# Kernel tuning notes

Measured on AMD Instinct MI355X. Metric: run time of the kernel, lower is better.

## Reference

```python
import jax, jax.numpy as jnp
import numpy as np

IMG_H = 800
IMG_W = 800
LEVEL_HW = [(200, 200), (100, 100), (50, 50), (25, 25), (13, 13)]
SIZES = [32.0, 64.0, 128.0, 256.0, 512.0]
RATIOS = np.array([0.5, 1.0, 2.0])
PRE_NMS = 1000     # rpn_pre_nms_top_n_test
POST_NMS = 1000    # rpn_post_nms_top_n_test
NMS_THRESH = 0.7
MIN_SIZE = 1e-3
BBOX_CLAMP = float(np.log(1000.0 / 16.0))  # torchvision BoxCoder clamp


def _make_anchors():
    """torchvision AnchorGenerator: 3 anchors/location, (h,w,a)-major order."""
    per_level = []
    for (H, W), size in zip(LEVEL_HW, SIZES):
        h_r = np.sqrt(RATIOS)
        w_r = 1.0 / h_r
        ws = w_r * size
        hs = h_r * size
        base = np.round(np.stack([-ws, -hs, ws, hs], axis=1) / 2.0)  # [3,4]
        stride_y = IMG_H // H
        stride_x = IMG_W // W
        shift_x = np.arange(W) * stride_x
        shift_y = np.arange(H) * stride_y
        yy, xx = np.meshgrid(shift_y, shift_x, indexing='ij')
        shifts = np.stack([xx.ravel(), yy.ravel(), xx.ravel(), yy.ravel()], axis=1)
        a = (shifts[:, None, :] + base[None, :, :]).reshape(-1, 4)  # [H*W*3,4]
        per_level.append(jnp.asarray(a, jnp.float32))
    return per_level


def _conv(x, w, b, pad):
    y = jax.lax.conv_general_dilated(
        x, w, window_strides=(1, 1), padding=[(pad, pad), (pad, pad)],
        dimension_numbers=('NCHW', 'OIHW', 'NCHW'))
    return y + b[None, :, None, None]


def _rpn_forward(feats, conv_w, conv_b, cls_w, cls_b, bbox_w, bbox_b):
    anchors_l = _make_anchors()
    boxes_list, scores_list, lvls_list = [], [], []
    for lvl, f in enumerate(feats):
        t = jax.nn.relu(_conv(f, conv_w, conv_b, 1))
        logits = _conv(t, cls_w, cls_b, 0)     # [1,3,H,W]
        deltas = _conv(t, bbox_w, bbox_b, 0)   # [1,12,H,W]
        H, W = f.shape[2], f.shape[3]
        s = logits[0].transpose(1, 2, 0).reshape(-1)                       # (h,w,a)
        d = deltas[0].reshape(3, 4, H, W).transpose(2, 3, 0, 1).reshape(-1, 4)
        k = min(PRE_NMS, s.shape[0])
        topv, topi = jax.lax.top_k(s, k)
        a = anchors_l[lvl][topi]
        dd = d[topi]
        # BoxCoder.decode, weights=(1,1,1,1)
        w_ = a[:, 2] - a[:, 0]
        h_ = a[:, 3] - a[:, 1]
        cx = a[:, 0] + 0.5 * w_
        cy = a[:, 1] + 0.5 * h_
        dx, dy = dd[:, 0], dd[:, 1]
        dw = jnp.minimum(dd[:, 2], BBOX_CLAMP)
        dh = jnp.minimum(dd[:, 3], BBOX_CLAMP)
        pcx = dx * w_ + cx
        pcy = dy * h_ + cy
        pw = jnp.exp(dw) * w_
        ph = jnp.exp(dh) * h_
        bx = jnp.stack([pcx - 0.5 * pw, pcy - 0.5 * ph,
                        pcx + 0.5 * pw, pcy + 0.5 * ph], axis=1)
        boxes_list.append(bx)
        scores_list.append(topv)
        lvls_list.append(jnp.full((k,), float(lvl), jnp.float32))
    boxes = jnp.concatenate(boxes_list)    # [N,4], N=4507
    scores = jnp.concatenate(scores_list)
    lvls = jnp.concatenate(lvls_list)
    # clip to image
    boxes = jnp.stack([boxes[:, 0].clip(0.0, IMG_W), boxes[:, 1].clip(0.0, IMG_H),
                       boxes[:, 2].clip(0.0, IMG_W), boxes[:, 3].clip(0.0, IMG_H)], axis=1)
    valid = ((boxes[:, 2] - boxes[:, 0]) >= MIN_SIZE) & ((boxes[:, 3] - boxes[:, 1]) >= MIN_SIZE)
    # batched NMS: offset boxes per level so cross-level IoU is zero
    off = lvls * (IMG_W + 1.0)
    ob = boxes + off[:, None]
    N = boxes.shape[0]
    order = jnp.argsort(-scores)
    b = ob[order]
    rb = boxes[order]
    s = scores[order]
    v = valid[order]
    area = (b[:, 2] - b[:, 0]) * (b[:, 3] - b[:, 1])
    lt = jnp.maximum(b[:, None, :2], b[None, :, :2])
    rbr = jnp.minimum(b[:, None, 2:], b[None, :, 2:])
    wh = jnp.clip(rbr - lt, 0.0)
    inter = wh[..., 0] * wh[..., 1]
    iou = inter / (area[:, None] + area[None, :] - inter)  # [N,N]
    idxs = jnp.arange(N)
    def body(i, keep):
        sup = keep[i] & (iou[i] > NMS_THRESH) & (idxs > i)
        return keep & ~sup
    keep = jax.lax.fori_loop(0, N, body, v)
    final_scores = jnp.where(keep, s, -jnp.inf)
    _, ki = jax.lax.top_k(final_scores, POST_NMS)
    return rb[ki]  # [POST_NMS, 4] proposals (padded to fixed size)


def setup_inputs() -> dict:
    key = jax.random.key(0)
    ks = jax.random.split(key, 12)
    inp = {}
    for i, (name, (H, W)) in enumerate(zip(['feat0', 'feat1', 'feat2', 'feat3', 'feat4'], LEVEL_HW)):
        inp[name] = jax.random.normal(ks[i], (1, 256, H, W), jnp.float32)
    inp['conv_w'] = jax.random.normal(ks[5], (256, 256, 3, 3), jnp.float32) * 0.02
    inp['conv_b'] = jnp.zeros((256,), jnp.float32)
    inp['cls_w'] = jax.random.normal(ks[6], (3, 256, 1, 1), jnp.float32) * 0.02
    inp['cls_b'] = jnp.zeros((3,), jnp.float32)
    inp['bbox_w'] = jax.random.normal(ks[7], (12, 256, 1, 1), jnp.float32) * 0.02
    inp['bbox_b'] = jnp.zeros((12,), jnp.float32)
    return inp


def reference(feat0, feat1, feat2, feat3, feat4, conv_w, conv_b, cls_w, cls_b, bbox_w, bbox_b):
    feats = [feat0, feat1, feat2, feat3, feat4]
    return _rpn_forward(feats, conv_w, conv_b, cls_w, cls_b, bbox_w, bbox_b)
```

## Files before the change

kernel.cpp:

```cpp
#include <hip/hip_runtime.h>
#include <cmath>

typedef unsigned int u32;
typedef unsigned long long u64;
typedef _Float16 f16;
typedef _Float16 f16x8 __attribute__((ext_vector_type(8)));
typedef float f32x4 __attribute__((ext_vector_type(4)));

typedef __attribute__((address_space(1))) const unsigned int gu32;
typedef __attribute__((address_space(3))) unsigned int lu32;

#define NCAND 4507
#define WORDS 71
#define ROWS_AL (WORDS * 64)
#define TOTS 159882

__constant__ int c_W[5]      = {200, 100, 50, 25, 13};
__constant__ int c_stride[5] = {4, 8, 16, 32, 61};
__constant__ int c_Nl[5]     = {120000, 30000, 7500, 1875, 507};
__constant__ int c_soff[5]   = {0, 120000, 150000, 157500, 159375};
__constant__ int c_k[5]      = {1000, 1000, 1000, 1000, 507};

__constant__ int cv_boff[6]  = {0, 625, 794, 843, 859, 863};

struct DecParams { float b[5][3][4]; };
struct FeatPtrs { const float* p[5]; };

__device__ __forceinline__ u32 flipf(float f) {
    u32 u = __float_as_uint(f);
    return (u & 0x80000000u) ? ~u : (u | 0x80000000u);
}

constexpr size_t AL(size_t x) { return (x + 255) & ~(size_t)255; }
constexpr size_t OFF_WHI    = 0;
constexpr size_t OFF_WLO    = AL(OFF_WHI + 1179648);
constexpr size_t OFF_HEADW  = AL(OFF_WLO + 1179648);
constexpr size_t OFF_HEADB  = AL(OFF_HEADW + 3840 * 4);
constexpr size_t OFF_SCORES = AL(OFF_HEADB + 64);
constexpr size_t OFF_DELTAS = AL(OFF_SCORES + (size_t)TOTS * 4);
constexpr size_t OFF_SBOX   = AL(OFF_DELTAS + (size_t)TOTS * 16);
constexpr size_t OFF_SOB    = AL(OFF_SBOX + (size_t)NCAND * 16);
constexpr size_t OFF_SVAL   = AL(OFF_SOB + (size_t)NCAND * 16);
constexpr size_t OFF_MASK   = AL(OFF_SVAL + (size_t)NCAND * 4);
constexpr size_t OFF_KEEP   = AL(OFF_MASK + (size_t)ROWS_AL * WORDS * 8);
constexpr size_t OFF_GHIST  = AL(OFF_KEEP + WORDS * 8);
constexpr size_t OFF_CNT    = AL(OFF_GHIST + 1280 * 4);
constexpr size_t OFF_KEY    = AL(OFF_CNT + 64);

__global__ __launch_bounds__(256) void k_prep(
    const float* __restrict__ cw, const float* __restrict__ clsw,
    const float* __restrict__ clsb, const float* __restrict__ bw,
    const float* __restrict__ bb, f16* __restrict__ whi, f16* __restrict__ wlo,
    float* __restrict__ headw, float* __restrict__ headb,
    u32* __restrict__ ghist, u32* __restrict__ cnts) {
    int i = blockIdx.x * 256 + threadIdx.x;
    if (i < 589824) {
        int blk = i >> 13;
        int within = i & 8191;
        int co = within >> 5;
        int rem = within & 31;
        int slot = rem >> 3, j = rem & 7;
        int chunk = blk / 9, kk = blk - chunk * 9;
        int ky = kk / 3, kx = kk - ky * 3;
        int g = slot ^ ((co >> 1) & 3);
        int ci = (chunk << 5) | (g << 3) | j;
        float w = cw[(((co << 8) + ci) * 3 + ky) * 3 + kx];
        f16 hi = (f16)w;
        whi[i] = hi;
        wlo[i] = (f16)((w - (float)hi) * 2048.0f);
    }
    if (i < 3840) {
        int h = i >> 8, ci = i & 255;
        headw[i] = (h < 3) ? clsw[h * 256 + ci] : bw[(h - 3) * 256 + ci];
    }
    if (i < 15) headb[i] = (i < 3) ? clsb[i] : bb[i - 3];
    if (i < 1280) ghist[i] = 0;
    if (i < 16) cnts[i] = 0;
}

__global__ __launch_bounds__(512) void k_conv(
    FeatPtrs fp, const f16* __restrict__ whi, const f16* __restrict__ wlo,
    const float* __restrict__ convb, const float* __restrict__ headw,
    const float* __restrict__ headb, float* __restrict__ scores,
    float* __restrict__ deltas) {
    __shared__ float4 smq[4896];
    char* smb = (char*)smq;
    const int tid = threadIdx.x;
    const int lane = tid & 63, wv = tid >> 6;
    const int l15 = lane & 15, l4 = lane >> 4;

    const int bid = blockIdx.x;
    int l = 0;
#pragma unroll
    for (int q = 1; q < 5; q++) if (bid >= cv_boff[q]) l = q;
    const int H = c_W[l], W = H;
    const int soff = c_soff[l];
    const float* __restrict__ in = fp.p[l];
    const int t = bid - cv_boff[l];
    const int tilesx = (W + 7) >> 3;
    const int tx = t % tilesx, ty = t / tilesx;
    const int x0 = tx * 8, y0 = ty * 8;
    const int HW = H * W;

    int rbase0, rbase1, rbase2, rbase3;
    {
        int rr = l15 >> 3;
        rbase0 = (0 + rr) * 640; rbase1 = (2 + rr) * 640;
        rbase2 = (4 + rr) * 640; rbase3 = (6 + rr) * 640;
    }
    int colx0, colx1, colx2;
    {
        int c = lane & 7;
        int p0 = c, p1 = c + 1, p2 = c + 2;
        colx0 = p0 * 64 + ((l4 ^ ((p0 >> 1) & 3)) << 4);
        colx1 = p1 * 64 + ((l4 ^ ((p1 >> 1) & 3)) << 4);
        colx2 = p2 * 64 + ((l4 ^ ((p2 >> 1) & 3)) << 4);
    }
    int bco0 = wv * 32 + l15, bco1 = wv * 32 + 16 + l15;
    const int boff0 = bco0 * 64 + ((l4 ^ ((bco0 >> 1) & 3)) << 4);
    const int boff1 = bco1 * 64 + ((l4 ^ ((bco1 >> 1) & 3)) << 4);

    f32x4 acc1[4][2], acc2[4][2];
#pragma unroll
    for (int mt = 0; mt < 4; mt++)
#pragma unroll
        for (int nt = 0; nt < 2; nt++) {
            acc1[mt][nt] = (f32x4)0.0f;
            acc2[mt][nt] = (f32x4)0.0f;
        }

    auto stagePatch = [&](int chunk) {
        const int c0 = chunk << 5;
        f16* ph = (f16*)smb;
        f16* pl = (f16*)(smb + 6400);
        for (int e = tid; e < 3200; e += 512) {
            int py = e / 320, rem = e - py * 320;
            int px = rem >> 5, ci = rem & 31;
            int gy = y0 - 1 + py, gx = x0 - 1 + px;
            float v = 0.f;
            if (gy >= 0 && gy < H && gx >= 0 && gx < W)
                v = in[(c0 + ci) * HW + gy * W + gx];
            f16 hi = (f16)v;
            int widx = py * 320 + px * 32 + (((ci >> 3) ^ ((px >> 1) & 3)) << 3) + (ci & 7);
            ph[widx] = hi;
            pl[widx] = (f16)((v - (float)hi) * 2048.0f);
        }
    };
    auto issueB = [&](int sidx, int buf) {
        const char* gh = (const char*)whi + (size_t)sidx * 16384;
        const char* gl = (const char*)wlo + (size_t)sidx * 16384;
        char* dh = smb + 12800 + buf * 32768;
        char* dl = dh + 16384;
#pragma unroll
        for (int q = 0; q < 2; q++) {
            int i1 = (wv * 2 + q) * 1024;
            __builtin_amdgcn_global_load_lds((gu32*)(gh + i1 + lane * 16), (lu32*)(dh + i1), 16, 0, 0);
            __builtin_amdgcn_global_load_lds((gu32*)(gl + i1 + lane * 16), (lu32*)(dl + i1), 16, 0, 0);
        }
    };

    stagePatch(0);
    issueB(0, 0);
    __syncthreads();

    for (int chunk = 0; chunk < 8; ++chunk) {
        if (chunk) { stagePatch(chunk); __syncthreads(); }
#pragma unroll
        for (int kk = 0; kk < 9; ++kk) {
            const int s = chunk * 9 + kk;
            const int buf = s & 1;
            if (s < 71) issueB(s + 1, buf ^ 1);
            {
                const int ky = kk / 3, kx = kk - ky * 3;
                const int kyb = ky * 640;
                const int cx = (kx == 0) ? colx0 : (kx == 1) ? colx1 : colx2;
                const char* bh = smb + 12800 + buf * 32768;
                const char* bl = bh + 16384;
                f16x8 ah0 = *(const f16x8*)(smb + rbase0 + kyb + cx);
                f16x8 ah1 = *(const f16x8*)(smb + rbase1 + kyb + cx);
                f16x8 ah2 = *(const f16x8*)(smb + rbase2 + kyb + cx);
                f16x8 ah3 = *(const f16x8*)(smb + rbase3 + kyb + cx);
                f16x8 al0 = *(const f16x8*)(smb + 6400 + rbase0 + kyb + cx);
                f16x8 al1 = *(const f16x8*)(smb + 6400 + rbase1 + kyb + cx);
                f16x8 al2 = *(const f16x8*)(smb + 6400 + rbase2 + kyb + cx);
                f16x8 al3 = *(const f16x8*)(smb + 6400 + rbase3 + kyb + cx);
#pragma unroll
                for (int nt = 0; nt < 2; nt++) {
                    const int bo = nt ? boff1 : boff0;
                    f16x8 vbh = *(const f16x8*)(bh + bo);
                    f16x8 vbl = *(const f16x8*)(bl + bo);
                    acc1[0][nt] = __builtin_amdgcn_mfma_f32_16x16x32_f16(ah0, vbh, acc1[0][nt], 0, 0, 0);
                    acc2[0][nt] = __builtin_amdgcn_mfma_f32_16x16x32_f16(ah0, vbl, acc2[0][nt], 0, 0, 0);
                    acc2[0][nt] = __builtin_amdgcn_mfma_f32_16x16x32_f16(al0, vbh, acc2[0][nt], 0, 0, 0);
                    acc1[1][nt] = __builtin_amdgcn_mfma_f32_16x16x32_f16(ah1, vbh, acc1[1][nt], 0, 0, 0);
                    acc2[1][nt] = __builtin_amdgcn_mfma_f32_16x16x32_f16(ah1, vbl, acc2[1][nt], 0, 0, 0);
                    acc2[1][nt] = __builtin_amdgcn_mfma_f32_16x16x32_f16(al1, vbh, acc2[1][nt], 0, 0, 0);
                    acc1[2][nt] = __builtin_amdgcn_mfma_f32_16x16x32_f16(ah2, vbh, acc1[2][nt], 0, 0, 0);
                    acc2[2][nt] = __builtin_amdgcn_mfma_f32_16x16x32_f16(ah2, vbl, acc2[2][nt], 0, 0, 0);
                    acc2[2][nt] = __builtin_amdgcn_mfma_f32_16x16x32_f16(al2, vbh, acc2[2][nt], 0, 0, 0);
                    acc1[3][nt] = __builtin_amdgcn_mfma_f32_16x16x32_f16(ah3, vbh, acc1[3][nt], 0, 0, 0);
                    acc2[3][nt] = __builtin_amdgcn_mfma_f32_16x16x32_f16(ah3, vbl, acc2[3][nt], 0, 0, 0);
                    acc2[3][nt] = __builtin_amdgcn_mfma_f32_16x16x32_f16(al3, vbh, acc2[3][nt], 0, 0, 0);
                }
            }
            __syncthreads();
        }
    }

    const float INV2048 = 4.8828125e-4f;
    {
        float cb0 = convb[bco0], cb1 = convb[bco1];
#pragma unroll
        for (int mt = 0; mt < 4; mt++)
#pragma unroll
            for (int nt = 0; nt < 2; nt++) {
                float cb = nt ? cb1 : cb0;
#pragma unroll
                for (int r = 0; r < 4; r++) {
                    float tv = acc1[mt][nt][r] + acc2[mt][nt][r] * INV2048 + cb;
                    acc1[mt][nt][r] = tv > 0.f ? tv : 0.f;
                }
            }
    }

    float* part = (float*)smb;
    for (int hc = 0; hc < 15; hc += 3) {
        float hw3[3][2];
#pragma unroll
        for (int h3 = 0; h3 < 3; h3++) {
            hw3[h3][0] = headw[(hc + h3) * 256 + bco0];
            hw3[h3][1] = headw[(hc + h3) * 256 + bco1];
        }
#pragma unroll
        for (int mt = 0; mt < 4; mt++)
#pragma unroll
            for (int r = 0; r < 4; r++) {
                float p0 = 0.f, p1 = 0.f, p2 = 0.f;
#pragma unroll
                for (int nt = 0; nt < 2; nt++) {
                    float tv = acc1[mt][nt][r];
                    p0 = fmaf(hw3[0][nt], tv, p0);
                    p1 = fmaf(hw3[1][nt], tv, p1);
                    p2 = fmaf(hw3[2][nt], tv, p2);
                }
                p0 += __shfl_xor(p0, 1); p0 += __shfl_xor(p0, 2); p0 += __shfl_xor(p0, 4); p0 += __shfl_xor(p0, 8);
                p1 += __shfl_xor(p1, 1); p1 += __shfl_xor(p1, 2); p1 += __shfl_xor(p1, 4); p1 += __shfl_xor(p1, 8);
                p2 += __shfl_xor(p2, 1); p2 += __shfl_xor(p2, 2); p2 += __shfl_xor(p2, 4); p2 += __shfl_xor(p2, 8);
                if (l15 == 0) {
                    int px = mt * 16 + l4 * 4 + r;
                    part[(wv * 64 + px) * 3 + 0] = p0;
                    part[(wv * 64 + px) * 3 + 1] = p1;
                    part[(wv * 64 + px) * 3 + 2] = p2;
                }
            }
        __syncthreads();
        if (tid < 192) {
            int px = tid / 3, h3 = tid % 3;
            int h = hc + h3;
            float sum = 0.f;
#pragma unroll
            for (int g = 0; g < 8; g++) sum += part[(g * 64 + px) * 3 + h3];
            sum += headb[h];
            int gy = y0 + (px >> 3), gx = x0 + (px & 7);
            if (gy < H && gx < W) {
                int pix = gy * W + gx;
                if (h < 3) {
                    scores[soff + pix * 3 + h] = sum;
                } else {
                    int ch2 = h - 3;
                    deltas[((size_t)(soff + pix * 3 + (ch2 >> 2))) * 4 + (ch2 & 3)] = sum;
                }
            }
        }
        __syncthreads();
    }
}

__global__ __launch_bounds__(256) void k_hist(
    const float* __restrict__ scores, u32* __restrict__ ghist) {
    __shared__ u32 lh[1280];
    for (int i = threadIdx.x; i < 1280; i += 256) lh[i] = 0;
    __syncthreads();
    const int gsz = gridDim.x * 256;
    for (int i = blockIdx.x * 256 + threadIdx.x; i < TOTS; i += gsz) {
        int l = (i >= 120000) + (i >= 150000) + (i >= 157500) + (i >= 159375);
        u32 b = flipf(scores[i]) >> 24;
        atomicAdd(&lh[l * 256 + b], 1u);
    }
    __syncthreads();
    for (int i = threadIdx.x; i < 1280; i += 256) {
        u32 v = lh[i];
        if (v) atomicAdd(&ghist[i], v);
    }
}

__global__ __launch_bounds__(512) void k_classify(
    const float* __restrict__ scores, const u32* __restrict__ ghist,
    u64* __restrict__ key, u64* __restrict__ scr1, u32* __restrict__ cnts) {
    __shared__ u32 lh[1280];
    __shared__ u32 sb0[5];
    for (int i = threadIdx.x; i < 1280; i += 512) lh[i] = ghist[i];
    __syncthreads();
    if (threadIdx.x < 4) {
        int l = threadIdx.x;
        u32 m0 = (u32)c_k[l];
        u32 cum = 0;
        for (int b = 255; b >= 0; --b) {
            u32 c = lh[l * 256 + b];
            if (cum + c >= m0) { sb0[l] = (u32)b; break; }
            cum += c;
        }
    }
    __syncthreads();
    const int lane = threadIdx.x & 63;
    const int gsz = gridDim.x * 512;
    for (int i = blockIdx.x * 512 + threadIdx.x; i < TOTS; i += gsz) {
        int l = (i >= 120000) + (i >= 150000) + (i >= 157500) + (i >= 159375);
        u32 il = (u32)(i - c_soff[l]);
        u32 k32 = flipf(scores[i]);
        u32 b = k32 >> 24;
        bool sel = (l == 4) || (b > sb0[l]);
        bool tie = (l < 4) && (b == sb0[l]);
        u64 m1 = __ballot(sel);
        while (m1) {
            int ldr = __builtin_ctzll(m1);
            int lv = __shfl(l, ldr);
            u64 grp = __ballot(sel && (l == lv));
            u32 bs = 0;
            if (lane == ldr) bs = atomicAdd(&cnts[lv], (u32)__popcll(grp));
            bs = __shfl(bs, ldr);
            if (sel && l == lv) {
                u32 slot = bs + (u32)__popcll(grp & ((1ull << lane) - 1ull));
                key[lv * 1000 + slot] = ((u64)(~k32) << 32) | (u64)(((u32)lv << 24) | il);
            }
            m1 &= ~grp;
        }
        u64 m2 = __ballot(tie);
        while (m2) {
            int ldr = __builtin_ctzll(m2);
            int lv = __shfl(l, ldr);
            u64 grp = __ballot(tie && (l == lv));
            u32 bs = 0;
            if (lane == ldr) bs = atomicAdd(&cnts[8 + lv], (u32)__popcll(grp));
            bs = __shfl(bs, ldr);
            if (tie && l == lv) {
                u32 slot = bs + (u32)__popcll(grp & ((1ull << lane) - 1ull));
                scr1[c_soff[lv] + slot] = ((u64)k32 << 32) | (u64)il;
            }
            m2 &= ~grp;
        }
    }
}

__global__ __launch_bounds__(1024) void k_finish(
    const u32* __restrict__ cnts, const u64* __restrict__ key,
    const float* __restrict__ deltas, DecParams P,
    u64* __restrict__ scr1, u64* __restrict__ scr2,
    float* __restrict__ sboxes, float* __restrict__ sob, u32* __restrict__ svalid) {
    __shared__ u64 sk[8192];
    __shared__ u32 hist[256];
    __shared__ u32 tiebuf[2048];
    __shared__ u32 sh_sel, sh_t1, sh_t2, sh_m;
    const int tid = threadIdx.x;
    const int lane = tid & 63;

    for (int l = 0; l < 5; ++l) {
        u32 n = cnts[l];
        int base = l * 1000;
        for (u32 j = tid; j < n; j += 1024) sk[base + j] = key[base + j];
    }
    __syncthreads();

    for (int l = 0; l < 4; ++l) {
        const int off = c_soff[l], base = l * 1000;
        const u32 lshift = (u32)l << 24;
        u32 nsel = cnts[l];
        u32 m = (u32)c_k[l] - nsel;
        u32 n = cnts[8 + l];
        u64* curb = scr1 + off;
        u64* nxtb = scr2 + off;
        if (tid == 0) sh_sel = nsel;
        __syncthreads();
        for (int p = 1; p <= 3; ++p) {
            if (n == m) break;
            const int shift = 56 - 8 * p;
            for (int b = tid; b < 256; b += 1024) hist[b] = 0;
            if (tid == 0) sh_t1 = 0;
            __syncthreads();
            for (u32 j = tid; j < n; j += 1024)
                atomicAdd(&hist[(u32)(curb[j] >> shift) & 255u], 1u);
            __syncthreads();
            if (tid == 0) {
                u32 cum = 0;
                for (int b = 255; b >= 0; --b) {
                    u32 c = hist[b];
                    if (cum + c >= m) { sh_t2 = (u32)b; sh_m = m - cum; break; }
                    cum += c;
                }
            }
            __syncthreads();
            u32 bp = sh_t2; m = sh_m;
            for (u32 j = tid; j < n; j += 1024) {
                u64 e = curb[j];
                u32 b = (u32)(e >> shift) & 255u;
                bool sel = b > bp, tie = (b == bp);
                u64 msk = __ballot(sel);
                if (msk) {
                    int ldr = __builtin_ctzll(msk);
                    u32 bs = 0;
                    if (lane == ldr) bs = atomicAdd(&sh_sel, (u32)__popcll(msk));
                    bs = __shfl(bs, ldr);
                    if (sel) {
                        u32 slot = bs + (u32)__popcll(msk & ((1ull << lane) - 1ull));
                        u32 k32 = (u32)(e >> 32);
                        sk[base + slot] = ((u64)(~k32) << 32) | (u64)(lshift | (u32)(e & 0xFFFFFFu));
                    }
                }
                msk = __ballot(tie);
                if (msk) {
                    int ldr = __builtin_ctzll(msk);
                    u32 bs = 0;
                    if (lane == ldr) bs = atomicAdd(&sh_t1, (u32)__popcll(msk));
                    bs = __shfl(bs, ldr);
                    if (tie) {
                        u32 slot = bs + (u32)__popcll(msk & ((1ull << lane) - 1ull));
                        nxtb[slot] = e;
                    }
                }
            }
            __syncthreads();
            n = sh_t1;
            __syncthreads();
            u64* tmp = curb; curb = nxtb; nxtb = tmp;
        }
        u32 cs = sh_sel;
        if (n == m) {
            for (u32 j = tid; j < n; j += 1024) {
                u64 e = curb[j];
                u32 k32 = (u32)(e >> 32);
                sk[base + cs + j] = ((u64)(~k32) << 32) | (u64)(lshift | (u32)(e & 0xFFFFFFu));
            }
        } else {
            u32 kt = (u32)(curb[0] >> 32);
            u32 nc = n > 2048u ? 2048u : n;
            u32 S = 64; while (S < nc) S <<= 1;
            for (u32 j = tid; j < S; j += 1024) tiebuf[j] = 0xFFFFFFFFu;
            __syncthreads();
            for (u32 j = tid; j < nc; j += 1024) tiebuf[j] = (u32)(curb[j] & 0xFFFFFFu);
            __syncthreads();
            for (u32 ksz = 2; ksz <= S; ksz <<= 1) {
                for (u32 jj = ksz >> 1; jj > 0; jj >>= 1) {
                    for (u32 i2 = tid; i2 < S; i2 += 1024) {
                        u32 ixj = i2 ^ jj;
                        if (ixj > i2) {
                            u32 a = tiebuf[i2], b2 = tiebuf[ixj];
                            bool up = ((i2 & ksz) == 0);
                            if ((a > b2) == up) { tiebuf[i2] = b2; tiebuf[ixj] = a; }
                        }
                    }
                    __syncthreads();
                }
            }
            for (u32 j = tid; j < m; j += 1024)
                sk[base + cs + j] = ((u64)(~kt) << 32) | (u64)(lshift | tiebuf[j]);
        }
        __syncthreads();
    }
    for (int i = tid; i < 8192; i += 1024) if (i >= NCAND) sk[i] = ~0ull;
    __syncthreads();
    for (u32 ksz = 2; ksz <= 8192; ksz <<= 1) {
        for (u32 j = ksz >> 1; j > 0; j >>= 1) {
            for (u32 i = tid; i < 8192; i += 1024) {
                u32 ixj = i ^ j;
                if (ixj > i) {
                    u64 a = sk[i], b = sk[ixj];
                    bool up = ((i & ksz) == 0);
                    if ((a > b) == up) { sk[i] = b; sk[ixj] = a; }
                }
            }
            __syncthreads();
        }
    }
    const float CLAMP = 4.135166556742356f;
    for (int s = tid; s < NCAND; s += 1024) {
        u32 info = (u32)sk[s];
        int l = info >> 24, idx = info & 0xFFFFFF;
        int W = c_W[l], st = c_stride[l];
        int a = idx % 3, pix = idx / 3;
        int x = pix % W, y = pix / W;
        float ax1 = x * st + P.b[l][a][0];
        float ay1 = y * st + P.b[l][a][1];
        float ax2 = x * st + P.b[l][a][2];
        float ay2 = y * st + P.b[l][a][3];
        float w_ = ax2 - ax1, h_ = ay2 - ay1;
        float cx = ax1 + 0.5f * w_, cy = ay1 + 0.5f * h_;
        const float* d = deltas + ((size_t)(c_soff[l] + idx)) * 4;
        float dx = d[0], dy = d[1];
        float dw = fminf(d[2], CLAMP), dh = fminf(d[3], CLAMP);
        float pcx = dx * w_ + cx, pcy = dy * h_ + cy;
        float pw = expf(dw) * w_, ph = expf(dh) * h_;
        float x1 = pcx - 0.5f * pw, y1 = pcy - 0.5f * ph;
        float x2 = pcx + 0.5f * pw, y2 = pcy + 0.5f * ph;
        x1 = fminf(fmaxf(x1, 0.f), 800.f); y1 = fminf(fmaxf(y1, 0.f), 800.f);
        x2 = fminf(fmaxf(x2, 0.f), 800.f); y2 = fminf(fmaxf(y2, 0.f), 800.f);
        u32 vv = (x2 - x1 >= 0.001f && y2 - y1 >= 0.001f) ? 1u : 0u;
        float offv = (float)l * 801.0f;
        sboxes[s * 4 + 0] = x1; sboxes[s * 4 + 1] = y1;
        sboxes[s * 4 + 2] = x2; sboxes[s * 4 + 3] = y2;
        sob[s * 4 + 0] = x1 + offv; sob[s * 4 + 1] = y1 + offv;
        sob[s * 4 + 2] = x2 + offv; sob[s * 4 + 3] = y2 + offv;
        svalid[s] = vv;
    }
}

__global__ __launch_bounds__(256) void k_mask(
    const float* __restrict__ sob, u64* __restrict__ mask) {
    int gid = blockIdx.x * 256 + threadIdx.x;
    const int total = NCAND * WORDS;
    if (gid >= total) return;
    int i = gid / WORDS, w = gid - i * WORDS;
    float bx1 = sob[i * 4], by1 = sob[i * 4 + 1], bx2 = sob[i * 4 + 2], by2 = sob[i * 4 + 3];
    float ai = (bx2 - bx1) * (by2 - by1);
    u64 bits = 0;
    int j0 = w * 64;
    for (int b = 0; b < 64; b++) {
        int j = j0 + b;
        if (j < NCAND && j > i) {
            float cx1 = sob[j * 4], cy1 = sob[j * 4 + 1], cx2 = sob[j * 4 + 2], cy2 = sob[j * 4 + 3];
            float lt0 = fmaxf(bx1, cx1), lt1 = fmaxf(by1, cy1);
            float rb0 = fminf(bx2, cx2), rb1 = fminf(by2, cy2);
            float ww = fmaxf(rb0 - lt0, 0.f), hh = fmaxf(rb1 - lt1, 0.f);
            float inter = ww * hh;
            float aj = (cx2 - cx1) * (cy2 - cy1);
            float u = ai + aj - inter;
            float iou = inter / u;
            if (iou > 0.7f) bits |= (1ull << b);
        }
    }
    mask[(size_t)i * WORDS + w] = bits;
}

__global__ __launch_bounds__(1024) void k_scan(
    const u64* __restrict__ mask, const u32* __restrict__ svalid,
    const float* __restrict__ sboxes, float* __restrict__ out) {
    __shared__ u64 keep[WORDS];
    __shared__ u32 ormL[WORDS], ormH[WORDS];
    __shared__ u32 sc[1024];
    const int tid = threadIdx.x;
    if (tid < WORDS) {
        u64 w0 = 0;
        for (int b = 0; b < 64; b++) {
            int idx = tid * 64 + b;
            if (idx < NCAND && svalid[idx]) w0 |= (1ull << b);
        }
        keep[tid] = w0; ormL[tid] = 0; ormH[tid] = 0;
    }
    __syncthreads();
    for (int t = 0; t < WORDS; t++) {
        if (tid < 64) {
            int row = t * 64 + tid;
            u64 d = (row < NCAND) ? mask[(size_t)row * WORDS + t] : 0ull;
            u32 dlo = (u32)d, dhi = (u32)(d >> 32);
            u64 cur = keep[t];
            u64 pending = cur;
            while (pending) {
                int b = __builtin_ctzll(pending);
                pending &= pending - 1;
                u64 mb = ((u64)__shfl(dhi, b, 64) << 32) | (u64)__shfl(dlo, b, 64);
                cur &= ~mb;
                pending &= ~mb;
            }
            if (tid == 0) keep[t] = cur;
        }
        __syncthreads();
        u64 kw = keep[t];
        int nW = WORDS - 1 - t;
        for (int task = tid; task < 64 * nW; task += 1024) {
            int r = task / nW, w = t + 1 + (task - r * nW);
            if ((kw >> r) & 1ull) {
                u64 mrow = mask[(size_t)(t * 64 + r) * WORDS + w];
                if (mrow) {
                    atomicOr(&ormL[w], (u32)mrow);
                    atomicOr(&ormH[w], (u32)(mrow >> 32));
                }
            }
        }
        __syncthreads();
        if (tid > t && tid < WORDS) {
            keep[tid] &= ~(((u64)ormH[tid] << 32) | (u64)ormL[tid]);
            ormL[tid] = 0; ormH[tid] = 0;
        }
        __syncthreads();
    }
    const int i0 = tid * 5;
    u32 cnt = 0;
    for (int e = 0; e < 5; e++) {
        int i = i0 + e;
        if (i < NCAND) cnt += (u32)((keep[i >> 6] >> (i & 63)) & 1ull);
    }
    sc[tid] = cnt;
    __syncthreads();
    for (int off = 1; off < 1024; off <<= 1) {
        u32 v = (tid >= off) ? sc[tid - off] : 0;
        __syncthreads();
        sc[tid] += v;
        __syncthreads();
    }
    u32 incl = sc[tid];
    u32 total = sc[1023];
    u32 kr = incl - cnt;
    for (int e = 0; e < 5; e++) {
        int i = i0 + e;
        if (i < NCAND) {
            bool kp = (keep[i >> 6] >> (i & 63)) & 1ull;
            if (kp) {
                if (kr < 1000u) {
                    out[kr * 4 + 0] = sboxes[i * 4 + 0];
                    out[kr * 4 + 1] = sboxes[i * 4 + 1];
                    out[kr * 4 + 2] = sboxes[i * 4 + 2];
                    out[kr * 4 + 3] = sboxes[i * 4 + 3];
                }
                kr++;
            } else {
                u32 slot = total + (u32)i - kr;
                if (slot < 1000u) {
                    out[slot * 4 + 0] = sboxes[i * 4 + 0];
                    out[slot * 4 + 1] = sboxes[i * 4 + 1];
                    out[slot * 4 + 2] = sboxes[i * 4 + 2];
                    out[slot * 4 + 3] = sboxes[i * 4 + 3];
                }
            }
        }
    }
}

extern "C" void kernel_launch(void* const* d_in, const int* in_sizes, int n_in,
                              void* d_out, int out_size, void* d_ws, size_t ws_size,
                              hipStream_t stream) {
    (void)in_sizes; (void)n_in; (void)out_size; (void)ws_size;
    FeatPtrs fp;
    for (int i = 0; i < 5; i++) fp.p[i] = (const float*)d_in[i];
    const float* conv_w = (const float*)d_in[5];
    const float* conv_b = (const float*)d_in[6];
    const float* cls_w  = (const float*)d_in[7];
    const float* cls_b  = (const float*)d_in[8];
    const float* bbox_w = (const float*)d_in[9];
    const float* bbox_b = (const float*)d_in[10];

    char* ws = (char*)d_ws;
    f16*   whi    = (f16*)(ws + OFF_WHI);
    f16*   wlo    = (f16*)(ws + OFF_WLO);
    float* headw  = (float*)(ws + OFF_HEADW);
    float* headb  = (float*)(ws + OFF_HEADB);
    float* scores = (float*)(ws + OFF_SCORES);
    float* deltas = (float*)(ws + OFF_DELTAS);
    float* sboxes = (float*)(ws + OFF_SBOX);
    float* sob    = (float*)(ws + OFF_SOB);
    u32*   svalid = (u32*)(ws + OFF_SVAL);
    u64*   maskp  = (u64*)(ws + OFF_MASK);
    u32*   ghist  = (u32*)(ws + OFF_GHIST);
    u32*   cnts   = (u32*)(ws + OFF_CNT);
    u64*   key    = (u64*)(ws + OFF_KEY);
    u64*   scr1   = maskp;
    u64*   scr2   = maskp + TOTS;

    k_prep<<<2304, 256, 0, stream>>>(conv_w, cls_w, cls_b, bbox_w, bbox_b,
                                     whi, wlo, headw, headb, ghist, cnts);

    k_conv<<<863, 512, 0, stream>>>(fp, whi, wlo, conv_b, headw, headb, scores, deltas);

    k_hist<<<256, 256, 0, stream>>>(scores, ghist);
    k_classify<<<320, 512, 0, stream>>>(scores, ghist, key, scr1, cnts);

    DecParams dp;
    {
        const double sz[5] = {32.0, 64.0, 128.0, 256.0, 512.0};
        const double rt[3] = {0.5, 1.0, 2.0};
        for (int l = 0; l < 5; l++)
            for (int a = 0; a < 3; a++) {
                double hr = sqrt(rt[a]);
                double wr = 1.0 / hr;
                double w = wr * sz[l], h = hr * sz[l];
                dp.b[l][a][0] = (float)nearbyint(-w / 2.0);
                dp.b[l][a][1] = (float)nearbyint(-h / 2.0);
                dp.b[l][a][2] = (float)nearbyint(w / 2.0);
                dp.b[l][a][3] = (float)nearbyint(h / 2.0);
            }
    }
    k_finish<<<1, 1024, 0, stream>>>(cnts, key, deltas, dp, scr1, scr2,
                                     sboxes, sob, svalid);
    k_mask<<<(NCAND * WORDS + 255) / 256, 256, 0, stream>>>(sob, maskp);
    k_scan<<<1, 1024, 0, stream>>>(maskp, svalid, sboxes, (float*)d_out);
}
```

Before: 986.5 us.

## Fuse histogram into conv, merge classify/finish and mask/scan via last-block pattern

The conv kernel becomes persistent, looping over the tiles from a fixed grid of blocks, and builds the score histogram in shared memory as it writes scores, which removes the separate histogram pass. The classify and finish kernels are merged, and so are the mask and scan kernels, with an atomic counter so the last block to finish runs the serial tail. The aim is to save kernel launches and an extra read of all scores. In exchange the conv now runs 863 tiles on 512 blocks, so some blocks do two tiles and finish late, and the counters in cnts[12] and cnts[13] must be zeroed before every call.

```diff
diff --git a/kernel.cpp b/kernel.cpp
--- a/kernel.cpp
+++ b/kernel.cpp
@@ -14,6 +14,8 @@
 #define WORDS 71
 #define ROWS_AL (WORDS * 64)
 #define TOTS 159882
+#define NTILES 863
+#define CONVGRID 512
 
 __constant__ int c_W[5]      = {200, 100, 50, 25, 13};
 __constant__ int c_stride[5] = {4, 8, 16, 32, 61};
@@ -82,25 +84,12 @@
     FeatPtrs fp, const f16* __restrict__ whi, const f16* __restrict__ wlo,
     const float* __restrict__ convb, const float* __restrict__ headw,
     const float* __restrict__ headb, float* __restrict__ scores,
-    float* __restrict__ deltas) {
+    float* __restrict__ deltas, u32* __restrict__ ghist) {
     __shared__ float4 smq[4896];
     char* smb = (char*)smq;
     const int tid = threadIdx.x;
     const int lane = tid & 63, wv = tid >> 6;
     const int l15 = lane & 15, l4 = lane >> 4;
-
-    const int bid = blockIdx.x;
-    int l = 0;
-#pragma unroll
-    for (int q = 1; q < 5; q++) if (bid >= cv_boff[q]) l = q;
-    const int H = c_W[l], W = H;
-    const int soff = c_soff[l];
-    const float* __restrict__ in = fp.p[l];
-    const int t = bid - cv_boff[l];
-    const int tilesx = (W + 7) >> 3;
-    const int tx = t % tilesx, ty = t / tilesx;
-    const int x0 = tx * 8, y0 = ty * 8;
-    const int HW = H * W;
 
     int rbase0, rbase1, rbase2, rbase3;
     {
@@ -116,193 +105,206 @@
         colx1 = p1 * 64 + ((l4 ^ ((p1 >> 1) & 3)) << 4);
         colx2 = p2 * 64 + ((l4 ^ ((p2 >> 1) & 3)) << 4);
     }
-    int bco0 = wv * 32 + l15, bco1 = wv * 32 + 16 + l15;
+    const int bco0 = wv * 32 + l15, bco1 = wv * 32 + 16 + l15;
     const int boff0 = bco0 * 64 + ((l4 ^ ((bco0 >> 1) & 3)) << 4);
     const int boff1 = bco1 * 64 + ((l4 ^ ((bco1 >> 1) & 3)) << 4);
 
-    f32x4 acc1[4][2], acc2[4][2];
-#pragma unroll
-    for (int mt = 0; mt < 4; mt++)
-#pragma unroll
-        for (int nt = 0; nt < 2; nt++) {
-            acc1[mt][nt] = (f32x4)0.0f;
-            acc2[mt][nt] = (f32x4)0.0f;
-        }
-
-    auto stagePatch = [&](int chunk) {
-        const int c0 = chunk << 5;
-        f16* ph = (f16*)smb;
-        f16* pl = (f16*)(smb + 6400);
-        for (int e = tid; e < 3200; e += 512) {
-            int py = e / 320, rem = e - py * 320;
-            int px = rem >> 5, ci = rem & 31;
-            int gy = y0 - 1 + py, gx = x0 - 1 + px;
-            float v = 0.f;
-            if (gy >= 0 && gy < H && gx >= 0 && gx < W)
-                v = in[(c0 + ci) * HW + gy * W + gx];
-            f16 hi = (f16)v;
-            int widx = py * 320 + px * 32 + (((ci >> 3) ^ ((px >> 1) & 3)) << 3) + (ci & 7);
-            ph[widx] = hi;
-            pl[widx] = (f16)((v - (float)hi) * 2048.0f);
-        }
-    };
-    auto issueB = [&](int sidx, int buf) {
-        const char* gh = (const char*)whi + (size_t)sidx * 16384;
-        const char* gl = (const char*)wlo + (size_t)sidx * 16384;
-        char* dh = smb + 12800 + buf * 32768;
-        char* dl = dh + 16384;
-#pragma unroll
-        for (int q = 0; q < 2; q++) {
-            int i1 = (wv * 2 + q) * 1024;
-            __builtin_amdgcn_global_load_lds((gu32*)(gh + i1 + lane * 16), (lu32*)(dh + i1), 16, 0, 0);
-            __builtin_amdgcn_global_load_lds((gu32*)(gl + i1 + lane * 16), (lu32*)(dl + i1), 16, 0, 0);
-        }
-    };
-
-    stagePatch(0);
-    issueB(0, 0);
-    __syncthreads();
-
-    for (int chunk = 0; chunk < 8; ++chunk) {
-        if (chunk) { stagePatch(chunk); __syncthreads(); }
-#pragma unroll
-        for (int kk = 0; kk < 9; ++kk) {
-            const int s = chunk * 9 + kk;
-            const int buf = s & 1;
-            if (s < 71) issueB(s + 1, buf ^ 1);
-            {
-                const int ky = kk / 3, kx = kk - ky * 3;
-                const int kyb = ky * 640;
-                const int cx = (kx == 0) ? colx0 : (kx == 1) ? colx1 : colx2;
-                const char* bh = smb + 12800 + buf * 32768;
-                const char* bl = bh + 16384;
-                f16x8 ah0 = *(const f16x8*)(smb + rbase0 + kyb + cx);
-                f16x8 ah1 = *(const f16x8*)(smb + rbase1 + kyb + cx);
-                f16x8 ah2 = *(const f16x8*)(smb + rbase2 + kyb + cx);
-                f16x8 ah3 = *(const f16x8*)(smb + rbase3 + kyb + cx);
-                f16x8 al0 = *(const f16x8*)(smb + 6400 + rbase0 + kyb + cx);
-                f16x8 al1 = *(const f16x8*)(smb + 6400 + rbase1 + kyb + cx);
-                f16x8 al2 = *(const f16x8*)(smb + 6400 + rbase2 + kyb + cx);
-                f16x8 al3 = *(const f16x8*)(smb + 6400 + rbase3 + kyb + cx);
+    for (int bt = blockIdx.x; bt < NTILES; bt += gridDim.x) {
+        int l = 0;
+#pragma unroll
+        for (int q = 1; q < 5; q++) if (bt >= cv_boff[q]) l = q;
+        const int H = c_W[l], W = H;
+        const int soff = c_soff[l];
+        const float* __restrict__ in = fp.p[l];
+        const int t = bt - cv_boff[l];
+        const int tilesx = (W + 7) >> 3;
+        const int tx = t % tilesx, ty = t / tilesx;
+        const int x0 = tx * 8, y0 = ty * 8;
+        const int HW = H * W;
+
+        f32x4 acc1[4][2], acc2[4][2];
+#pragma unroll
+        for (int mt = 0; mt < 4; mt++)
+#pragma unroll
+            for (int nt = 0; nt < 2; nt++) {
+                acc1[mt][nt] = (f32x4)0.0f;
+                acc2[mt][nt] = (f32x4)0.0f;
+            }
+
+        auto stagePatch = [&](int chunk) {
+            const int c0 = chunk << 5;
+            f16* ph = (f16*)smb;
+            f16* pl = (f16*)(smb + 6400);
+            for (int e = tid; e < 3200; e += 512) {
+                int py = e / 320, rem = e - py * 320;
+                int px = rem >> 5, ci = rem & 31;
+                int gy = y0 - 1 + py, gx = x0 - 1 + px;
+                float v = 0.f;
+                if (gy >= 0 && gy < H && gx >= 0 && gx < W)
+                    v = in[(c0 + ci) * HW + gy * W + gx];
+                f16 hi = (f16)v;
+                int widx = py * 320 + px * 32 + (((ci >> 3) ^ ((px >> 1) & 3)) << 3) + (ci & 7);
+                ph[widx] = hi;
+                pl[widx] = (f16)((v - (float)hi) * 2048.0f);
+            }
+        };
+        auto issueB = [&](int sidx, int buf) {
+            const char* gh = (const char*)whi + (size_t)sidx * 16384;
+            const char* gl = (const char*)wlo + (size_t)sidx * 16384;
+            char* dh = smb + 12800 + buf * 32768;
+            char* dl = dh + 16384;
+#pragma unroll
+            for (int q = 0; q < 2; q++) {
+                int i1 = (wv * 2 + q) * 1024;
+                __builtin_amdgcn_global_load_lds((gu32*)(gh + i1 + lane * 16), (lu32*)(dh + i1), 16, 0, 0);
+                __builtin_amdgcn_global_load_lds((gu32*)(gl + i1 + lane * 16), (lu32*)(dl + i1), 16, 0, 0);
+            }
+        };
+
+        stagePatch(0);
+        issueB(0, 0);
+        __syncthreads();
+
+        for (int chunk = 0; chunk < 8; ++chunk) {
+            if (chunk) { stagePatch(chunk); __syncthreads(); }
+#pragma unroll
+            for (int kk = 0; kk < 9; ++kk) {
+                const int s = chunk * 9 + kk;
+                const int buf = s & 1;
+                if (s < 71) issueB(s + 1, buf ^ 1);
+                {
+                    const int ky = kk / 3, kx = kk - ky * 3;
+                    const int kyb = ky * 640;
+                    const int cx = (kx == 0) ? colx0 : (kx == 1) ? colx1 : colx2;
+                    const char* bh = smb + 12800 + buf * 32768;
+                    const char* bl = bh + 16384;
+                    f16x8 ah0 = *(const f16x8*)(smb + rbase0 + kyb + cx);
+                    f16x8 ah1 = *(const f16x8*)(smb + rbase1 + kyb + cx);
+                    f16x8 ah2 = *(const f16x8*)(smb + rbase2 + kyb + cx);
+                    f16x8 ah3 = *(const f16x8*)(smb + rbase3 + kyb + cx);
+                    f16x8 al0 = *(const f16x8*)(smb + 6400 + rbase0 + kyb + cx);
+                    f16x8 al1 = *(const f16x8*)(smb + 6400 + rbase1 + kyb + cx);
+                    f16x8 al2 = *(const f16x8*)(smb + 6400 + rbase2 + kyb + cx);
+                    f16x8 al3 = *(const f16x8*)(smb + 6400 + rbase3 + kyb + cx);
+#pragma unroll
+                    for (int nt = 0; nt < 2; nt++) {
+                        const int bo = nt ? boff1 : boff0;
+                        f16x8 vbh = *(const f16x8*)(bh + bo);
+                        f16x8 vbl = *(const f16x8*)(bl + bo);
+                        acc1[0][nt] = __builtin_amdgcn_mfma_f32_16x16x32_f16(ah0, vbh, acc1[0][nt], 0, 0, 0);
+                        acc2[0][nt] = __builtin_amdgcn_mfma_f32_16x16x32_f16(ah0, vbl, acc2[0][nt], 0, 0, 0);
+                        acc2[0][nt] = __builtin_amdgcn_mfma_f32_16x16x32_f16(al0, vbh, acc2[0][nt], 0, 0, 0);
+                        acc1[1][nt] = __builtin_amdgcn_mfma_f32_16x16x32_f16(ah1, vbh, acc1[1][nt], 0, 0, 0);
+                        acc2[1][nt] = __builtin_amdgcn_mfma_f32_16x16x32_f16(ah1, vbl, acc2[1][nt], 0, 0, 0);
+                        acc2[1][nt] = __builtin_amdgcn_mfma_f32_16x16x32_f16(al1, vbh, acc2[1][nt], 0, 0, 0);
+                        acc1[2][nt] = __builtin_amdgcn_mfma_f32_16x16x32_f16(ah2, vbh, acc1[2][nt], 0, 0, 0);
+                        acc2[2][nt] = __builtin_amdgcn_mfma_f32_16x16x32_f16(ah2, vbl, acc2[2][nt], 0, 0, 0);
+                        acc2[2][nt] = __builtin_amdgcn_mfma_f32_16x16x32_f16(al2, vbh, acc2[2][nt], 0, 0, 0);
+                        acc1[3][nt] = __builtin_amdgcn_mfma_f32_16x16x32_f16(ah3, vbh, acc1[3][nt], 0, 0, 0);
+                        acc2[3][nt] = __builtin_amdgcn_mfma_f32_16x16x32_f16(ah3, vbl, acc2[3][nt], 0, 0, 0);
+                        acc2[3][nt] = __builtin_amdgcn_mfma_f32_16x16x32_f16(al3, vbh, acc2[3][nt], 0, 0, 0);
+                    }
+                }
+                __syncthreads();
+            }
+        }
+
+        const float INV2048 = 4.8828125e-4f;
+        {
+            float cb0 = convb[bco0], cb1 = convb[bco1];
+#pragma unroll
+            for (int mt = 0; mt < 4; mt++)
 #pragma unroll
                 for (int nt = 0; nt < 2; nt++) {
-                    const int bo = nt ? boff1 : boff0;
-                    f16x8 vbh = *(const f16x8*)(bh + bo);
-                    f16x8 vbl = *(const f16x8*)(bl + bo);
-                    acc1[0][nt] = __builtin_amdgcn_mfma_f32_16x16x32_f16(ah0, vbh, acc1[0][nt], 0, 0, 0);
-                    acc2[0][nt] = __builtin_amdgcn_mfma_f32_16x16x32_f16(ah0, vbl, acc2[0][nt], 0, 0, 0);
-                    acc2[0][nt] = __builtin_amdgcn_mfma_f32_16x16x32_f16(al0, vbh, acc2[0][nt], 0, 0, 0);
-                    acc1[1][nt] = __builtin_amdgcn_mfma_f32_16x16x32_f16(ah1, vbh, acc1[1][nt], 0, 0, 0);
-                    acc2[1][nt] = __builtin_amdgcn_mfma_f32_16x16x32_f16(ah1, vbl, acc2[1][nt], 0, 0, 0);
-                    acc2[1][nt] = __builtin_amdgcn_mfma_f32_16x16x32_f16(al1, vbh, acc2[1][nt], 0, 0, 0);
-                    acc1[2][nt] = __builtin_amdgcn_mfma_f32_16x16x32_f16(ah2, vbh, acc1[2][nt], 0, 0, 0);
-                    acc2[2][nt] = __builtin_amdgcn_mfma_f32_16x16x32_f16(ah2, vbl, acc2[2][nt], 0, 0, 0);
-                    acc2[2][nt] = __builtin_amdgcn_mfma_f32_16x16x32_f16(al2, vbh, acc2[2][nt], 0, 0, 0);
-                    acc1[3][nt] = __builtin_amdgcn_mfma_f32_16x16x32_f16(ah3, vbh, acc1[3][nt], 0, 0, 0);
-                    acc2[3][nt] = __builtin_amdgcn_mfma_f32_16x16x32_f16(ah3, vbl, acc2[3][nt], 0, 0, 0);
-                    acc2[3][nt] = __builtin_amdgcn_mfma_f32_16x16x32_f16(al3, vbh, acc2[3][nt], 0, 0, 0);
-                }
-            }
-            __syncthreads();
-        }
-    }
-
-    const float INV2048 = 4.8828125e-4f;
-    {
-        float cb0 = convb[bco0], cb1 = convb[bco1];
-#pragma unroll
-        for (int mt = 0; mt < 4; mt++)
-#pragma unroll
-            for (int nt = 0; nt < 2; nt++) {
-                float cb = nt ? cb1 : cb0;
+                    float cb = nt ? cb1 : cb0;
+#pragma unroll
+                    for (int r = 0; r < 4; r++) {
+                        float tv = acc1[mt][nt][r] + acc2[mt][nt][r] * INV2048 + cb;
+                        acc1[mt][nt][r] = tv > 0.f ? tv : 0.f;
+                    }
+                }
+        }
+
+        u32* lhist = (u32*)(smb + 12800);
+        for (int i = tid; i < 1280; i += 512) lhist[i] = 0;
+
+        float* part = (float*)smb;
+        for (int hc = 0; hc < 15; hc += 3) {
+            float hw3[3][2];
+#pragma unroll
+            for (int h3 = 0; h3 < 3; h3++) {
+                hw3[h3][0] = headw[(hc + h3) * 256 + bco0];
+                hw3[h3][1] = headw[(hc + h3) * 256 + bco1];
+            }
+#pragma unroll
+            for (int mt = 0; mt < 4; mt++)
 #pragma unroll
                 for (int r = 0; r < 4; r++) {
-                    float tv = acc1[mt][nt][r] + acc2[mt][nt][r] * INV2048 + cb;
-                    acc1[mt][nt][r] = tv > 0.f ? tv : 0.f;
-                }
-            }
-    }
-
-    float* part = (float*)smb;
-    for (int hc = 0; hc < 15; hc += 3) {
-        float hw3[3][2];
-#pragma unroll
-        for (int h3 = 0; h3 < 3; h3++) {
-            hw3[h3][0] = headw[(hc + h3) * 256 + bco0];
-            hw3[h3][1] = headw[(hc + h3) * 256 + bco1];
-        }
-#pragma unroll
-        for (int mt = 0; mt < 4; mt++)
-#pragma unroll
-            for (int r = 0; r < 4; r++) {
-                float p0 = 0.f, p1 = 0.f, p2 = 0.f;
-#pragma unroll
-                for (int nt = 0; nt < 2; nt++) {
-                    float tv = acc1[mt][nt][r];
-                    p0 = fmaf(hw3[0][nt], tv, p0);
-                    p1 = fmaf(hw3[1][nt], tv, p1);
-                    p2 = fmaf(hw3[2][nt], tv, p2);
-                }
-                p0 += __shfl_xor(p0, 1); p0 += __shfl_xor(p0, 2); p0 += __shfl_xor(p0, 4); p0 += __shfl_xor(p0, 8);
-                p1 += __shfl_xor(p1, 1); p1 += __shfl_xor(p1, 2); p1 += __shfl_xor(p1, 4); p1 += __shfl_xor(p1, 8);
-                p2 += __shfl_xor(p2, 1); p2 += __shfl_xor(p2, 2); p2 += __shfl_xor(p2, 4); p2 += __shfl_xor(p2, 8);
-                if (l15 == 0) {
-                    int px = mt * 16 + l4 * 4 + r;
-                    part[(wv * 64 + px) * 3 + 0] = p0;
-                    part[(wv * 64 + px) * 3 + 1] = p1;
-                    part[(wv * 64 + px) * 3 + 2] = p2;
-                }
-            }
-        __syncthreads();
-        if (tid < 192) {
-            int px = tid / 3, h3 = tid % 3;
-            int h = hc + h3;
-            float sum = 0.f;
-#pragma unroll
-            for (int g = 0; g < 8; g++) sum += part[(g * 64 + px) * 3 + h3];
-            sum += headb[h];
-            int gy = y0 + (px >> 3), gx = x0 + (px & 7);
-            if (gy < H && gx < W) {
-                int pix = gy * W + gx;
-                if (h < 3) {
-                    scores[soff + pix * 3 + h] = sum;
-                } else {
-                    int ch2 = h - 3;
-                    deltas[((size_t)(soff + pix * 3 + (ch2 >> 2))) * 4 + (ch2 & 3)] = sum;
-                }
-            }
+                    float p0 = 0.f, p1 = 0.f, p2 = 0.f;
+#pragma unroll
+                    for (int nt = 0; nt < 2; nt++) {
+                        float tv = acc1[mt][nt][r];
+                        p0 = fmaf(hw3[0][nt], tv, p0);
+                        p1 = fmaf(hw3[1][nt], tv, p1);
+                        p2 = fmaf(hw3[2][nt], tv, p2);
+                    }
+                    p0 += __shfl_xor(p0, 1); p0 += __shfl_xor(p0, 2); p0 += __shfl_xor(p0, 4); p0 += __shfl_xor(p0, 8);
+                    p1 += __shfl_xor(p1, 1); p1 += __shfl_xor(p1, 2); p1 += __shfl_xor(p1, 4); p1 += __shfl_xor(p1, 8);
+                    p2 += __shfl_xor(p2, 1); p2 += __shfl_xor(p2, 2); p2 += __shfl_xor(p2, 4); p2 += __shfl_xor(p2, 8);
+                    if (l15 == 0) {
+                        int px = mt * 16 + l4 * 4 + r;
+                        part[(wv * 64 + px) * 3 + 0] = p0;
+                        part[(wv * 64 + px) * 3 + 1] = p1;
+                        part[(wv * 64 + px) * 3 + 2] = p2;
+                    }
+                }
+            __syncthreads();
+            if (tid < 192) {
+                int px = tid / 3, h3 = tid % 3;
+                int h = hc + h3;
+                float sum = 0.f;
+#pragma unroll
+                for (int g = 0; g < 8; g++) sum += part[(g * 64 + px) * 3 + h3];
+                sum += headb[h];
+                int gy = y0 + (px >> 3), gx = x0 + (px & 7);
+                if (gy < H && gx < W) {
+                    int pix = gy * W + gx;
+                    if (h < 3) {
+                        scores[soff + pix * 3 + h] = sum;
+                        atomicAdd(&lhist[l * 256 + (flipf(sum) >> 24)], 1u);
+                    } else {
+                        int ch2 = h - 3;
+                        deltas[((size_t)(soff + pix * 3 + (ch2 >> 2))) * 4 + (ch2 & 3)] = sum;
+                    }
+                }
+            }
+            __syncthreads();
+        }
+        for (int i = tid; i < 1280; i += 512) {
+            u32 v = lhist[i];
+            if (v) atomicAdd(&ghist[i], v);
         }
         __syncthreads();
     }
 }
 
-__global__ __launch_bounds__(256) void k_hist(
-    const float* __restrict__ scores, u32* __restrict__ ghist) {
+__global__ __launch_bounds__(1024) void k_clsfin(
+    const float* __restrict__ scores, const u32* __restrict__ ghist,
+    u64* __restrict__ key, u64* __restrict__ scr1, u64* __restrict__ scr2,
+    u32* __restrict__ cnts, const float* __restrict__ deltas, DecParams P,
+    float* __restrict__ sboxes, float* __restrict__ sob, u32* __restrict__ svalid) {
+    __shared__ u64 sk[8192];
     __shared__ u32 lh[1280];
-    for (int i = threadIdx.x; i < 1280; i += 256) lh[i] = 0;
-    __syncthreads();
-    const int gsz = gridDim.x * 256;
-    for (int i = blockIdx.x * 256 + threadIdx.x; i < TOTS; i += gsz) {
-        int l = (i >= 120000) + (i >= 150000) + (i >= 157500) + (i >= 159375);
-        u32 b = flipf(scores[i]) >> 24;
-        atomicAdd(&lh[l * 256 + b], 1u);
-    }
-    __syncthreads();
-    for (int i = threadIdx.x; i < 1280; i += 256) {
-        u32 v = lh[i];
-        if (v) atomicAdd(&ghist[i], v);
-    }
-}
-
-__global__ __launch_bounds__(512) void k_classify(
-    const float* __restrict__ scores, const u32* __restrict__ ghist,
-    u64* __restrict__ key, u64* __restrict__ scr1, u32* __restrict__ cnts) {
-    __shared__ u32 lh[1280];
+    __shared__ u32 tiebuf[2048];
     __shared__ u32 sb0[5];
-    for (int i = threadIdx.x; i < 1280; i += 512) lh[i] = ghist[i];
-    __syncthreads();
-    if (threadIdx.x < 4) {
-        int l = threadIdx.x;
+    __shared__ u32 sh_sel, sh_t1, sh_t2, sh_m, sh_last;
+    const int tid = threadIdx.x;
+    const int lane = tid & 63;
+
+    for (int i = tid; i < 1280; i += 1024) lh[i] = ghist[i];
+    __syncthreads();
+    if (tid < 4) {
+        int l = tid;
         u32 m0 = (u32)c_k[l];
         u32 cum = 0;
         for (int b = 255; b >= 0; --b) {
@@ -312,9 +314,8 @@
         }
     }
     __syncthreads();
-    const int lane = threadIdx.x & 63;
-    const int gsz = gridDim.x * 512;
-    for (int i = blockIdx.x * 512 + threadIdx.x; i < TOTS; i += gsz) {
+    const int gsz = gridDim.x * 1024;
+    for (int i = blockIdx.x * 1024 + tid; i < TOTS; i += gsz) {
         int l = (i >= 120000) + (i >= 150000) + (i >= 157500) + (i >= 159375);
         u32 il = (u32)(i - c_soff[l]);
         u32 k32 = flipf(scores[i]);
@@ -350,27 +351,19 @@
             m2 &= ~grp;
         }
     }
-}
-
-__global__ __launch_bounds__(1024) void k_finish(
-    const u32* __restrict__ cnts, const u64* __restrict__ key,
-    const float* __restrict__ deltas, DecParams P,
-    u64* __restrict__ scr1, u64* __restrict__ scr2,
-    float* __restrict__ sboxes, float* __restrict__ sob, u32* __restrict__ svalid) {
-    __shared__ u64 sk[8192];
-    __shared__ u32 hist[256];
-    __shared__ u32 tiebuf[2048];
-    __shared__ u32 sh_sel, sh_t1, sh_t2, sh_m;
-    const int tid = threadIdx.x;
-    const int lane = tid & 63;
-
+    __threadfence();
+    if (tid == 0) sh_last = (atomicAdd(&cnts[12], 1u) == gridDim.x - 1) ? 1u : 0u;
+    __syncthreads();
+    if (!sh_last) return;
+    __threadfence();
+
+    u32* hist = lh;
     for (int l = 0; l < 5; ++l) {
         u32 n = cnts[l];
         int base = l * 1000;
         for (u32 j = tid; j < n; j += 1024) sk[base + j] = key[base + j];
     }
     __syncthreads();
-
     for (int l = 0; l < 4; ++l) {
         const int off = c_soff[l], base = l * 1000;
         const u32 lshift = (u32)l << 24;
@@ -513,40 +506,45 @@
     }
 }
 
-__global__ __launch_bounds__(256) void k_mask(
-    const float* __restrict__ sob, u64* __restrict__ mask) {
-    int gid = blockIdx.x * 256 + threadIdx.x;
-    const int total = NCAND * WORDS;
-    if (gid >= total) return;
-    int i = gid / WORDS, w = gid - i * WORDS;
-    float bx1 = sob[i * 4], by1 = sob[i * 4 + 1], bx2 = sob[i * 4 + 2], by2 = sob[i * 4 + 3];
-    float ai = (bx2 - bx1) * (by2 - by1);
-    u64 bits = 0;
-    int j0 = w * 64;
-    for (int b = 0; b < 64; b++) {
-        int j = j0 + b;
-        if (j < NCAND && j > i) {
-            float cx1 = sob[j * 4], cy1 = sob[j * 4 + 1], cx2 = sob[j * 4 + 2], cy2 = sob[j * 4 + 3];
-            float lt0 = fmaxf(bx1, cx1), lt1 = fmaxf(by1, cy1);
-            float rb0 = fminf(bx2, cx2), rb1 = fminf(by2, cy2);
-            float ww = fmaxf(rb0 - lt0, 0.f), hh = fmaxf(rb1 - lt1, 0.f);
-            float inter = ww * hh;
-            float aj = (cx2 - cx1) * (cy2 - cy1);
-            float u = ai + aj - inter;
-            float iou = inter / u;
-            if (iou > 0.7f) bits |= (1ull << b);
-        }
-    }
-    mask[(size_t)i * WORDS + w] = bits;
-}
-
-__global__ __launch_bounds__(1024) void k_scan(
-    const u64* __restrict__ mask, const u32* __restrict__ svalid,
-    const float* __restrict__ sboxes, float* __restrict__ out) {
+__global__ __launch_bounds__(1024) void k_maskscan(
+    const float* __restrict__ sob, u64* __restrict__ mask,
+    const u32* __restrict__ svalid, const float* __restrict__ sboxes,
+    float* __restrict__ out, u32* __restrict__ cnts) {
     __shared__ u64 keep[WORDS];
     __shared__ u32 ormL[WORDS], ormH[WORDS];
     __shared__ u32 sc[1024];
+    __shared__ u32 sh_last;
     const int tid = threadIdx.x;
+    int gid = blockIdx.x * 1024 + tid;
+    const int total = NCAND * WORDS;
+    if (gid < total) {
+        int i = gid / WORDS, w = gid - i * WORDS;
+        float bx1 = sob[i * 4], by1 = sob[i * 4 + 1], bx2 = sob[i * 4 + 2], by2 = sob[i * 4 + 3];
+        float ai = (bx2 - bx1) * (by2 - by1);
+        u64 bits = 0;
+        int j0 = w * 64;
+        for (int b = 0; b < 64; b++) {
+            int j = j0 + b;
+            if (j < NCAND && j > i) {
+                float cx1 = sob[j * 4], cy1 = sob[j * 4 + 1], cx2 = sob[j * 4 + 2], cy2 = sob[j * 4 + 3];
+                float lt0 = fmaxf(bx1, cx1), lt1 = fmaxf(by1, cy1);
+                float rb0 = fminf(bx2, cx2), rb1 = fminf(by2, cy2);
+                float ww = fmaxf(rb0 - lt0, 0.f), hh = fmaxf(rb1 - lt1, 0.f);
+                float inter = ww * hh;
+                float aj = (cx2 - cx1) * (cy2 - cy1);
+                float u = ai + aj - inter;
+                float iou = inter / u;
+                if (iou > 0.7f) bits |= (1ull << b);
+            }
+        }
+        mask[(size_t)i * WORDS + w] = bits;
+    }
+    __threadfence();
+    if (tid == 0) sh_last = (atomicAdd(&cnts[13], 1u) == gridDim.x - 1) ? 1u : 0u;
+    __syncthreads();
+    if (!sh_last) return;
+    __threadfence();
+
     if (tid < WORDS) {
         u64 w0 = 0;
         for (int b = 0; b < 64; b++) {
@@ -607,7 +605,7 @@
         __syncthreads();
     }
     u32 incl = sc[tid];
-    u32 total = sc[1023];
+    u32 totalk = sc[1023];
     u32 kr = incl - cnt;
     for (int e = 0; e < 5; e++) {
         int i = i0 + e;
@@ -622,7 +620,7 @@
                 }
                 kr++;
             } else {
-                u32 slot = total + (u32)i - kr;
+                u32 slot = totalk + (u32)i - kr;
                 if (slot < 1000u) {
                     out[slot * 4 + 0] = sboxes[i * 4 + 0];
                     out[slot * 4 + 1] = sboxes[i * 4 + 1];
@@ -667,10 +665,8 @@
     k_prep<<<2304, 256, 0, stream>>>(conv_w, cls_w, cls_b, bbox_w, bbox_b,
                                      whi, wlo, headw, headb, ghist, cnts);
 
-    k_conv<<<863, 512, 0, stream>>>(fp, whi, wlo, conv_b, headw, headb, scores, deltas);
-
-    k_hist<<<256, 256, 0, stream>>>(scores, ghist);
-    k_classify<<<320, 512, 0, stream>>>(scores, ghist, key, scr1, cnts);
+    k_conv<<<CONVGRID, 512, 0, stream>>>(fp, whi, wlo, conv_b, headw, headb,
+                                         scores, deltas, ghist);
 
     DecParams dp;
     {
@@ -687,8 +683,8 @@
                 dp.b[l][a][3] = (float)nearbyint(h / 2.0);
             }
     }
-    k_finish<<<1, 1024, 0, stream>>>(cnts, key, deltas, dp, scr1, scr2,
-                                     sboxes, sob, svalid);
-    k_mask<<<(NCAND * WORDS + 255) / 256, 256, 0, stream>>>(sob, maskp);
-    k_scan<<<1, 1024, 0, stream>>>(maskp, svalid, sboxes, (float*)d_out);
+    k_clsfin<<<128, 1024, 0, stream>>>(scores, ghist, key, scr1, scr2, cnts,
+                                       deltas, dp, sboxes, sob, svalid);
+    k_maskscan<<<(NCAND * WORDS + 1023) / 1024, 1024, 0, stream>>>(
+        sob, maskp, svalid, sboxes, (float*)d_out, cnts);
 }
```

Result: slower. 1.085 ms (+10.0%).
